# Optimization experiments

Hardware: AMD Instinct MI355X
Metric: run time of the kernel (lower is better)

The kernel has to match this reference:

```python
import jax, jax.numpy as jnp
import numpy as np

B, S, E, D, H, L = 128, 50, 512, 1024, 16, 4
V, NU, NF, NR = 100000, 50000, 10000, 5
DK = D // H
FF = 4 * D


def _pe(S, D):
    # FranchisePositionalEncoding: two interleaved sin/cos halves (chrono + release*1.5)
    half = D // 2
    pos = jnp.arange(S, dtype=jnp.float32)[:, None]
    div = jnp.exp(jnp.arange(0, half, 2, dtype=jnp.float32) * (-np.log(10000.0) / half))
    def il(a):
        return jnp.stack([jnp.sin(a), jnp.cos(a)], axis=-1).reshape(S, half)
    return jnp.concatenate([il(pos * div), il(pos * div * 1.5)], axis=-1)  # [S, D]


def _ln(x, g, b):
    m = x.mean(-1, keepdims=True)
    v = ((x - m) ** 2).mean(-1, keepdims=True)
    return (x - m) * jax.lax.rsqrt(v + 1e-5) * g + b


def _gelu(x):
    return jax.nn.gelu(x, approximate=False)


def setup_inputs() -> dict:
    key = jax.random.key(0)
    ks = iter(jax.random.split(key, 64))
    def p(shape, s=0.02):
        return jax.random.normal(next(ks), shape, jnp.float32) * s
    inp = {
        'movie_table': p((V, E)), 'fran_table': p((NF, E)), 'entry_table': p((NR, E)),
        'proj_w': p((3 * E, D)), 'proj_b': jnp.zeros((D,), jnp.float32),
        'wq': p((L, D, D)), 'bq': jnp.zeros((L, D), jnp.float32),
        'wk': p((L, D, D)), 'bk': jnp.zeros((L, D), jnp.float32),
        'wv': p((L, D, D)), 'bv': jnp.zeros((L, D), jnp.float32),
        'wo': p((L, D, D)), 'bo': jnp.zeros((L, D), jnp.float32),
        'rel_table': p((L, NR, DK)),
        'aln_g': jnp.ones((L, D), jnp.float32), 'aln_b': jnp.zeros((L, D), jnp.float32),
        'f_w1': p((L, D, FF)), 'f_b1': jnp.zeros((L, FF), jnp.float32),
        'f_w2': p((L, FF, D)), 'f_b2': jnp.zeros((L, D), jnp.float32),
        'ln_g': jnp.ones((L, D), jnp.float32), 'ln_b': jnp.zeros((L, D), jnp.float32),
        'user_table': p((NU, D)),
        'mq_w': p((D, D)), 'mq_b': jnp.zeros((D,), jnp.float32),
        'mk_w': p((D, D)), 'mk_b': jnp.zeros((D,), jnp.float32),
        'mv_w': p((D, D)), 'mv_b': jnp.zeros((D,), jnp.float32),
        'mo_w': p((D, D)), 'mo_b': jnp.zeros((D,), jnp.float32),
        'c_w1': p((2 * D, D)), 'c_b1': jnp.zeros((D,), jnp.float32),
        'c_w2': p((D, 1)), 'c_b2': jnp.zeros((1,), jnp.float32),
        'n_w1': p((2 * D, D)), 'n_b1': jnp.zeros((D,), jnp.float32),
        'n_w2': p((D, V)), 'n_b2': jnp.zeros((V,), jnp.float32),
        'r_w1': p((3 * D, D)), 'r_b1': jnp.zeros((D,), jnp.float32),
        'r_w2': p((D, 1)), 'r_b2': jnp.zeros((1,), jnp.float32),
        'o_w1': p((D, D // 2)), 'o_b1': jnp.zeros((D // 2,), jnp.float32),
        'o_w2': p((D // 2, 2)), 'o_b2': jnp.zeros((2,), jnp.float32),
        'user_ids': jax.random.randint(next(ks), (B,), 0, NU),
        'movie_ids': jax.random.randint(next(ks), (B, S), 0, V),
        'franchise_ids': jax.random.randint(next(ks), (B, S), 0, NF),
        'entry_types': jax.random.randint(next(ks), (B, S), 0, NR),
        'relation_matrix': jax.random.randint(next(ks), (S, S), 0, NR),
    }
    return inp


def reference(movie_table, fran_table, entry_table, proj_w, proj_b,
              wq, bq, wk, bk, wv, bv, wo, bo, rel_table, aln_g, aln_b,
              f_w1, f_b1, f_w2, f_b2, ln_g, ln_b, user_table,
              mq_w, mq_b, mk_w, mk_b, mv_w, mv_b, mo_w, mo_b,
              c_w1, c_b1, c_w2, c_b2, n_w1, n_b1, n_w2, n_b2,
              r_w1, r_b1, r_w2, r_b2, o_w1, o_b1, o_w2, o_b2,
              user_ids, movie_ids, franchise_ids, entry_types, relation_matrix):
    b, s = movie_ids.shape
    d = proj_w.shape[1]
    nl, _, dk = rel_table.shape
    h = d // dk
    scale = 1.0 / np.sqrt(dk).astype(np.float32)

    # encoder input: concat(movie, franchise, entry) embeddings -> proj -> +PE
    x = jnp.concatenate([movie_table[movie_ids], fran_table[franchise_ids],
                         entry_table[entry_types]], axis=-1) @ proj_w + proj_b
    x = x + _pe(s, d)

    for l in range(nl):
        res = x
        q = (x @ wq[l] + bq[l]).reshape(b, s, h, dk).transpose(0, 2, 1, 3)  # [b,h,s,dk]
        k = (x @ wk[l] + bk[l]).reshape(b, s, h, dk).transpose(0, 2, 1, 3)
        v = (x @ wv[l] + bv[l]).reshape(b, s, h, dk).transpose(0, 2, 1, 3)
        scores = jnp.einsum('bhid,bhjd->bhij', q, k) * scale
        rel = rel_table[l][relation_matrix]  # [s,s,dk]
        scores = scores + 0.5 * jnp.einsum('bhid,ijd->bhij', q, rel)
        attn = jax.nn.softmax(scores, axis=-1)
        ctx = jnp.einsum('bhij,bhjd->bhid', attn, v).transpose(0, 2, 1, 3).reshape(b, s, d)
        x = _ln(ctx @ wo[l] + bo[l] + res, aln_g[l], aln_b[l])
        ff = _gelu(x @ f_w1[l] + f_b1[l]) @ f_w2[l] + f_b2[l]
        x = _ln(x + ff, ln_g[l], ln_b[l])

    # user preference cross-attention (nn.MultiheadAttention, q_len=1)
    user_emb = user_table[user_ids]  # [b,d]
    qh = (user_emb @ mq_w + mq_b).reshape(b, h, dk)
    kh = (x @ mk_w + mk_b).reshape(b, s, h, dk)
    vh = (x @ mv_w + mv_b).reshape(b, s, h, dk)
    a = jax.nn.softmax(jnp.einsum('bhd,bshd->bhs', qh, kh) * scale, axis=-1)
    user_pref = jnp.einsum('bhs,bshd->bhd', a, vh).reshape(b, d) @ mo_w + mo_b

    seq_repr = x.mean(axis=1)  # mask is None path
    ci = jnp.concatenate([user_pref, seq_repr], axis=-1)
    completion = jax.nn.sigmoid(_gelu(ci @ c_w1 + c_b1) @ c_w2 + c_b2)
    next_logits = _gelu(ci @ n_w1 + n_b1) @ n_w2 + n_b2
    ri = jnp.concatenate([user_emb, user_pref, seq_repr], axis=-1)
    rating = _gelu(ri @ r_w1 + r_b1) @ r_w2 + r_b2
    order = jax.nn.softmax(_gelu(user_pref @ o_w1 + o_b1) @ o_w2 + o_b2, axis=-1)
    return (x, completion, next_logits, rating, order, user_pref)
```

## Files before the change

kernel.cpp:

```cpp
#include <hip/hip_runtime.h>
#include <hip/hip_bf16.h>
#include <math.h>

#define B_   128
#define S_   50
#define BS_  (B_*S_)
#define E_   512
#define D_   1024
#define H_   16
#define DK_  64
#define L_   4
#define FF_  4096
#define V_   100000

typedef short bf8_t __attribute__((ext_vector_type(8)));
typedef float f32x4 __attribute__((ext_vector_type(4)));
typedef unsigned short u16;

__device__ __forceinline__ float gelu_exact(float x) {
    return 0.5f * x * (1.0f + erff(x * 0.70710678118654752440f));
}
__device__ __forceinline__ u16 f2bf(float f) {
    unsigned int u = __float_as_uint(f);
    return (u16)((u + 0x7FFFu + ((u >> 16) & 1u)) >> 16);
}
__device__ __forceinline__ float bf2f(u16 u) {
    return __uint_as_float(((unsigned int)u) << 16);
}

__device__ __forceinline__ void gload16(const u16* g, u16* l) {
    auto* g1 = reinterpret_cast<const __attribute__((address_space(1))) unsigned int*>(
                   reinterpret_cast<uintptr_t>(g));
    auto* l3 = reinterpret_cast<__attribute__((address_space(3))) unsigned int*>(
                   reinterpret_cast<uintptr_t>(l));
    __builtin_amdgcn_global_load_lds(g1, l3, 16, 0, 0);
}

__device__ __forceinline__ void wtrans_body(
    const float* __restrict__ W, u16* __restrict__ Wt,
    int K, int N, int nb, int kb, int dstRowOff)
{
    __shared__ float t[32][33];
    int c = threadIdx.x & 31, r0 = threadIdx.x >> 5;
    #pragma unroll
    for (int rr = 0; rr < 32; rr += 8)
        t[rr + r0][c] = W[(size_t)(kb + rr + r0) * N + nb + c];
    __syncthreads();
    #pragma unroll
    for (int rr = 0; rr < 32; rr += 8)
        Wt[(size_t)(dstRowOff + nb + rr + r0) * K + kb + c] = f2bf(t[c][rr + r0]);
}

__global__ __launch_bounds__(256) void wtrans(
    const float* __restrict__ W, u16* __restrict__ Wt,
    int K, int N, long srcLS, long dstLS, int dstRowOff)
{
    int l = blockIdx.z;
    wtrans_body(W + (size_t)l * srcLS, Wt + (size_t)l * dstLS,
                K, N, blockIdx.x * 32, blockIdx.y * 32, dstRowOff);
}

__global__ __launch_bounds__(256) void wtrans_qkv(
    const float* __restrict__ wq, const float* __restrict__ wk, const float* __restrict__ wv,
    u16* __restrict__ dst)
{
    int z = blockIdx.z;
    int l = z & 3, which = z >> 2;
    const float* W = (which == 0 ? wq : which == 1 ? wk : wv) + (size_t)l * (D_ * D_);
    u16* Wt = dst + (size_t)l * (3 * D_ * D_) + (size_t)which * (D_ * D_);
    wtrans_body(W, Wt, D_, D_, blockIdx.x * 32, blockIdx.y * 32, 0);
}

struct WT8 { const float* s[8]; u16* d[8]; };
__global__ __launch_bounds__(256) void wtrans8(WT8 p)
{
    int z = blockIdx.z;
    wtrans_body(p.s[z], p.d[z], D_, D_, blockIdx.x * 32, blockIdx.y * 32, 0);
}

__global__ __launch_bounds__(256) void wtrans_ff(
    const float* __restrict__ w1, const float* __restrict__ w2,
    u16* __restrict__ d1, u16* __restrict__ d2)
{
    if (blockIdx.z == 0)
        wtrans_body(w1, d1, D_, FF_, blockIdx.x * 32, blockIdx.y * 32, 0);
    else
        wtrans_body(w2, d2, FF_, D_, blockIdx.y * 32, blockIdx.x * 32, 0);
}

__global__ __launch_bounds__(256) void embed_concat(
    const float* __restrict__ mt, const float* __restrict__ ft, const float* __restrict__ et,
    const int* __restrict__ mids, const int* __restrict__ fids, const int* __restrict__ eids,
    u16* __restrict__ xinb)
{
    int bs = blockIdx.x;
    int mid = mids[bs], fid = fids[bs], eid = eids[bs];
    const float* srcs[3] = { mt + (size_t)mid * E_, ft + (size_t)fid * E_, et + (size_t)eid * E_ };
    u16* dst = xinb + (size_t)bs * (3 * E_);
    for (int i = threadIdx.x; i < 384; i += 256) {
        int seg = i >> 7, off = i & 127;
        float4 v = reinterpret_cast<const float4*>(srcs[seg])[off];
        ushort4 b;
        b.x = f2bf(v.x); b.y = f2bf(v.y); b.z = f2bf(v.z); b.w = f2bf(v.w);
        reinterpret_cast<ushort4*>(dst + seg * E_)[off] = b;
    }
}

__global__ __launch_bounds__(256) void setup_misc(
    const float* __restrict__ bq, const float* __restrict__ bk, const float* __restrict__ bv,
    const float* __restrict__ cb1, const float* __restrict__ nb1,
    const float* __restrict__ mkb, const float* __restrict__ mvb,
    float* __restrict__ bqkv, float* __restrict__ bcn, float* __restrict__ bkv,
    float* __restrict__ pet)
{
    int bi = blockIdx.x, tid = threadIdx.x;
    if (bi < 4) {
        for (int c = tid; c < 3072; c += 256) {
            float v = (c < 1024) ? bq[bi * 1024 + c]
                    : (c < 2048) ? bk[bi * 1024 + c - 1024]
                                 : bv[bi * 1024 + c - 2048];
            bqkv[bi * 3072 + c] = v;
        }
    } else if (bi == 4) {
        for (int c = tid; c < 2048; c += 256)
            bcn[c] = (c < 1024) ? cb1[c] : nb1[c - 1024];
    } else if (bi == 5) {
        for (int c = tid; c < 2048; c += 256)
            bkv[c] = (c < 1024) ? mkb[c] : mvb[c - 1024];
    } else {
        int s = bi - 6;
        const float cc = -logf(10000.0f) / 512.0f;
        for (int d = tid; d < D_; d += 256) {
            int second = d >= 512;
            int c2 = second ? d - 512 : d;
            int i = c2 >> 1;
            float div = expf(cc * (float)(2 * i));
            float aa = (float)s * div * (second ? 1.5f : 1.0f);
            pet[s * D_ + d] = (c2 & 1) ? cosf(aa) : sinf(aa);
        }
    }
}

template<int BM>
__global__ __launch_bounds__(256) void gemm_bf16_t(
    const u16* __restrict__ A, int lda, const u16* __restrict__ Wt,
    const float* __restrict__ bias, float* __restrict__ Cf,
    u16* __restrict__ Cb, int ldcb, u16* __restrict__ Cb2, int ldcb2,
    int N, int K, int act, const float* __restrict__ pe)
{
    constexpr int MR   = BM / 32;
    constexpr int AL   = BM / 64;
    constexpr int ABUF = BM * 32;
    __shared__ u16 As[2 * ABUF];
    __shared__ u16 Bs[2 * 4096];
    const int tid  = threadIdx.x;
    const int lane = tid & 63;
    const int wid  = tid >> 6;
    const int wr   = wid >> 1, wc = wid & 1;

    const int gx  = gridDim.x;
    const int nwg = gx * gridDim.y;
    int orig = blockIdx.y * gx + blockIdx.x;
    int qq = nwg >> 3, rr2 = nwg & 7, xcd = orig & 7, idx = orig >> 3;
    int wgid = (xcd < rr2) ? (xcd * (qq + 1) + idx)
                           : (rr2 * (qq + 1) + (xcd - rr2) * qq + idx);
    const int rowBase = (wgid / gx) * BM;
    const int colBase = (wgid % gx) * 128;

    const int fr = lane & 15;
    const int hi = lane >> 4;

    const int sRowL  = lane >> 2;
    const int sChunk = lane & 3;
    const int aRow0 = wid * (BM / 4) + sRowL;
    const int aKey  = (aRow0 >> 1) & 3;
    const u16* aS0 = A + (size_t)(rowBase + aRow0) * lda + ((sChunk ^ aKey) << 3);
    const u16* aS1 = aS0 + (size_t)16 * lda;
    const int ldsA0 = (wid * (BM / 4)) * 32;
    const int ldsA1 = ldsA0 + 512;
    const int bRow0 = wid * 32 + sRowL;
    const int bKey  = (bRow0 >> 1) & 3;
    const u16* bS0 = Wt + (size_t)(colBase + bRow0) * K + ((sChunk ^ bKey) << 3);
    const u16* bS1 = bS0 + (size_t)16 * K;
    const int ldsB0 = (wid * 32) * 32;
    const int ldsB1 = ldsB0 + 512;

    const int swz = ((hi ^ ((fr >> 1) & 3)) << 3);
    const int aRd = (wr * (BM / 2) + fr) * 32 + swz;
    const int bRd = (wc * 64 + fr) * 32 + swz;

    f32x4 acc[MR][4] = {};
    const int nk = K >> 5;

    auto STAGE = [&](int kb, int buf) {
        u16* dA = As + buf * ABUF;
        u16* dB = Bs + buf * 4096;
        gload16(aS0 + kb, dA + ldsA0);
        if constexpr (AL == 2) gload16(aS1 + kb, dA + ldsA1);
        gload16(bS0 + kb, dB + ldsB0);
        gload16(bS1 + kb, dB + ldsB1);
    };

    STAGE(0, 0);
    __builtin_amdgcn_sched_barrier(0);
    STAGE(32, 1);
    __builtin_amdgcn_sched_barrier(0);
    if constexpr (BM == 128) asm volatile("s_waitcnt vmcnt(4)\n\ts_barrier" ::: "memory");
    else                     asm volatile("s_waitcnt vmcnt(3)\n\ts_barrier" ::: "memory");
    __builtin_amdgcn_sched_barrier(0);

    for (int t = 0; t < nk; ++t) {
        const int cur = t & 1;
        const u16* bA = As + cur * ABUF;
        const u16* bB = Bs + cur * 4096;
        bf8_t af[MR], bf[4];
        #pragma unroll
        for (int m = 0; m < MR; ++m)
            af[m] = *reinterpret_cast<const bf8_t*>(&bA[aRd + m * 512]);
        #pragma unroll
        for (int n = 0; n < 4; ++n)
            bf[n] = *reinterpret_cast<const bf8_t*>(&bB[bRd + n * 512]);
        #pragma unroll
        for (int m = 0; m < MR; ++m)
            #pragma unroll
            for (int n = 0; n < 4; ++n)
                acc[m][n] = __builtin_amdgcn_mfma_f32_16x16x32_bf16(af[m], bf[n], acc[m][n], 0, 0, 0);
        if (t == nk - 1) break;
        __builtin_amdgcn_sched_barrier(0);
        asm volatile("s_waitcnt lgkmcnt(0)\n\ts_barrier" ::: "memory");
        __builtin_amdgcn_sched_barrier(0);
        if (t + 2 < nk) {
            STAGE((t + 2) << 5, cur);
            __builtin_amdgcn_sched_barrier(0);
            if constexpr (BM == 128) asm volatile("s_waitcnt vmcnt(4)\n\ts_barrier" ::: "memory");
            else                     asm volatile("s_waitcnt vmcnt(3)\n\ts_barrier" ::: "memory");
        } else {
            asm volatile("s_waitcnt vmcnt(0)\n\ts_barrier" ::: "memory");
        }
        __builtin_amdgcn_sched_barrier(0);
    }

    const int orow = hi << 2;
    #pragma unroll
    for (int m = 0; m < MR; ++m) {
        int r0 = rowBase + wr * (BM / 2) + m * 16 + orow;
        #pragma unroll
        for (int n = 0; n < 4; ++n) {
            int c = colBase + wc * 64 + n * 16 + fr;
            float bv = bias ? bias[c] : 0.0f;
            #pragma unroll
            for (int r = 0; r < 4; ++r) {
                float v = acc[m][n][r] + bv;
                if (act == 1) v = gelu_exact(v);
                if (pe) v += pe[(size_t)((r0 + r) % S_) * N + c];
                if (Cf)  Cf [(size_t)(r0 + r) * N + c] = v;
                if (Cb)  Cb [(size_t)(r0 + r) * ldcb  + c] = f2bf(v);
                if (Cb2) Cb2[(size_t)(r0 + r) * ldcb2 + c] = f2bf(v);
            }
        }
    }
}

__global__ __launch_bounds__(256) void gemm_sk(
    const u16* __restrict__ A, int lda, const u16* __restrict__ Wt, int ldb,
    float* __restrict__ P0, float* __restrict__ P1,
    int N, int Kh)
{
    __shared__ u16 As[2 * 4096];
    __shared__ u16 Bs[2 * 4096];
    const int tid  = threadIdx.x;
    const int lane = tid & 63;
    const int wid  = tid >> 6;
    const int wr   = wid >> 1, wc = wid & 1;

    const int gx  = gridDim.x;
    const int nwg = gx * gridDim.y;
    int orig = blockIdx.y * gx + blockIdx.x;
    int qq = nwg >> 3, rr2 = nwg & 7, xcd = orig & 7, idx = orig >> 3;
    int wgid = (xcd < rr2) ? (xcd * (qq + 1) + idx)
                           : (rr2 * (qq + 1) + (xcd - rr2) * qq + idx);
    const int rowBase = (wgid / gx) * 128;
    const int colBase = (wgid % gx) * 128;
    const int k0 = blockIdx.z * Kh;
    float* P = blockIdx.z ? P1 : P0;

    const int fr = lane & 15;
    const int hi = lane >> 4;

    const int sRowL  = lane >> 2;
    const int sChunk = lane & 3;
    const int gRow0  = (wid << 5) + sRowL;
    const int skey   = (gRow0 >> 1) & 3;
    const int gC     = (sChunk ^ skey) << 3;
    const u16* aS0 = A  + (size_t)(rowBase + gRow0) * lda + k0 + gC;
    const u16* aS1 = aS0 + (size_t)16 * lda;
    const u16* bS0 = Wt + (size_t)(colBase + gRow0) * ldb + k0 + gC;
    const u16* bS1 = bS0 + (size_t)16 * ldb;
    const int ldsW0 = (wid << 5) << 5;
    const int ldsW1 = ldsW0 + (16 << 5);

    const int swz = ((hi ^ ((fr >> 1) & 3)) << 3);
    const int aRd = (wr * 64 + fr) * 32 + swz;
    const int bRd = (wc * 64 + fr) * 32 + swz;

    f32x4 acc[4][4] = {};
    const int nk = Kh >> 5;

    auto STAGE = [&](int kb, int buf) {
        u16* dA = As + buf * 4096;
        u16* dB = Bs + buf * 4096;
        gload16(aS0 + kb, dA + ldsW0);
        gload16(aS1 + kb, dA + ldsW1);
        gload16(bS0 + kb, dB + ldsW0);
        gload16(bS1 + kb, dB + ldsW1);
    };

    STAGE(0, 0);
    __builtin_amdgcn_sched_barrier(0);
    STAGE(32, 1);
    __builtin_amdgcn_sched_barrier(0);
    asm volatile("s_waitcnt vmcnt(4)\n\ts_barrier" ::: "memory");
    __builtin_amdgcn_sched_barrier(0);

    for (int t = 0; t < nk; ++t) {
        const int cur = t & 1;
        const u16* bA = As + cur * 4096;
        const u16* bB = Bs + cur * 4096;
        bf8_t af[4], bf[4];
        #pragma unroll
        for (int m = 0; m < 4; ++m)
            af[m] = *reinterpret_cast<const bf8_t*>(&bA[aRd + m * 512]);
        #pragma unroll
        for (int n = 0; n < 4; ++n)
            bf[n] = *reinterpret_cast<const bf8_t*>(&bB[bRd + n * 512]);
        #pragma unroll
        for (int m = 0; m < 4; ++m)
            #pragma unroll
            for (int n = 0; n < 4; ++n)
                acc[m][n] = __builtin_amdgcn_mfma_f32_16x16x32_bf16(af[m], bf[n], acc[m][n], 0, 0, 0);
        if (t == nk - 1) break;
        __builtin_amdgcn_sched_barrier(0);
        asm volatile("s_waitcnt lgkmcnt(0)\n\ts_barrier" ::: "memory");
        __builtin_amdgcn_sched_barrier(0);
        if (t + 2 < nk) {
            STAGE((t + 2) << 5, cur);
            __builtin_amdgcn_sched_barrier(0);
            asm volatile("s_waitcnt vmcnt(4)\n\ts_barrier" ::: "memory");
        } else {
            asm volatile("s_waitcnt vmcnt(0)\n\ts_barrier" ::: "memory");
        }
        __builtin_amdgcn_sched_barrier(0);
    }

    const int orow = hi << 2;
    #pragma unroll
    for (int m = 0; m < 4; ++m) {
        int r0 = rowBase + wr * 64 + m * 16 + orow;
        #pragma unroll
        for (int n = 0; n < 4; ++n) {
            int c = colBase + wc * 64 + n * 16 + fr;
            #pragma unroll
            for (int r = 0; r < 4; ++r)
                P[(size_t)(r0 + r) * N + c] = acc[m][n][r];
        }
    }
}

__global__ __launch_bounds__(256) void combine_bias_pe(
    const float* __restrict__ p1, const float* __restrict__ p2,
    const float* __restrict__ bias, const float* __restrict__ pe,
    u16* __restrict__ outb)
{
    int row = blockIdx.x, tid = threadIdx.x;
    int c0 = tid << 2;
    size_t base = (size_t)row * D_ + c0;
    float4 v1 = *reinterpret_cast<const float4*>(p1 + base);
    float4 v2 = *reinterpret_cast<const float4*>(p2 + base);
    float4 bv = *reinterpret_cast<const float4*>(bias + c0);
    float4 pv = *reinterpret_cast<const float4*>(pe + (size_t)(row % S_) * D_ + c0);
    ushort4 ob;
    ob.x = f2bf(v1.x + v2.x + bv.x + pv.x);
    ob.y = f2bf(v1.y + v2.y + bv.y + pv.y);
    ob.z = f2bf(v1.z + v2.z + bv.z + pv.z);
    ob.w = f2bf(v1.w + v2.w + bv.w + pv.w);
    *reinterpret_cast<ushort4*>(outb + base) = ob;
}

__global__ __launch_bounds__(256) void add_ln2(
    const float* __restrict__ p1, const float* __restrict__ p2,
    const float* __restrict__ bias, const u16* __restrict__ res,
    const float* __restrict__ g, const float* __restrict__ be,
    u16* __restrict__ outb, float* __restrict__ outf)
{
    int row = blockIdx.x, tid = threadIdx.x;
    int c0 = tid << 2;
    size_t base = (size_t)row * D_ + c0;
    float4 v1 = *reinterpret_cast<const float4*>(p1 + base);
    float4 v2 = *reinterpret_cast<const float4*>(p2 + base);
    float4 bv = *reinterpret_cast<const float4*>(bias + c0);
    ushort4 vr = *reinterpret_cast<const ushort4*>(res + base);
    float vals[4] = { v1.x + v2.x + bv.x + bf2f(vr.x),
                      v1.y + v2.y + bv.y + bf2f(vr.y),
                      v1.z + v2.z + bv.z + bf2f(vr.z),
                      v1.w + v2.w + bv.w + bf2f(vr.w) };
    float s = vals[0] + vals[1] + vals[2] + vals[3];
    __shared__ float red[8];
    #pragma unroll
    for (int off = 32; off; off >>= 1) s += __shfl_xor(s, off);
    int wave = tid >> 6, lane = tid & 63;
    if (lane == 0) red[wave] = s;
    __syncthreads();
    float mean = (red[0] + red[1] + red[2] + red[3]) * (1.0f / D_);
    float vv = 0.0f;
    #pragma unroll
    for (int t = 0; t < 4; ++t) {
        float d = vals[t] - mean;
        vv += d * d;
    }
    #pragma unroll
    for (int off = 32; off; off >>= 1) vv += __shfl_xor(vv, off);
    if (lane == 0) red[4 + wave] = vv;
    __syncthreads();
    float var = (red[4] + red[5] + red[6] + red[7]) * (1.0f / D_);
    float rstd = rsqrtf(var + 1e-5f);
    float4 gv  = *reinterpret_cast<const float4*>(g  + c0);
    float4 bev = *reinterpret_cast<const float4*>(be + c0);
    float o0 = (vals[0] - mean) * rstd * gv.x + bev.x;
    float o1 = (vals[1] - mean) * rstd * gv.y + bev.y;
    float o2 = (vals[2] - mean) * rstd * gv.z + bev.z;
    float o3 = (vals[3] - mean) * rstd * gv.w + bev.w;
    ushort4 ob;
    ob.x = f2bf(o0); ob.y = f2bf(o1); ob.z = f2bf(o2); ob.w = f2bf(o3);
    *reinterpret_cast<ushort4*>(outb + base) = ob;
    if (outf) {
        float4 of = { o0, o1, o2, o3 };
        *reinterpret_cast<float4*>(outf + base) = of;
    }
}

__global__ __launch_bounds__(256) void gemm_logits(
    const float* __restrict__ A, int lda, const float* __restrict__ W,
    const float* __restrict__ bias, float* __restrict__ C, int N, int K)
{
    __shared__ u16 As[2][128][40];
    __shared__ u16 Bs[2][128][40];
    const int tid  = threadIdx.x;
    const int lane = tid & 63;
    const int wid  = tid >> 6;
    const int wr   = wid >> 1, wc = wid & 1;
    const int colBase = blockIdx.x * 128;

    const int a_r = tid >> 1;
    const int a_h = (tid & 1) << 4;
    const int b_c = tid & 127;
    const int b_h = (tid >> 7) << 4;

    const int fr = lane & 15;
    const int fk = (lane >> 4) << 3;

    f32x4 acc[4][4] = {};
    const int nvalid = N - colBase;
    const bool valid = b_c < nvalid;
    const int nk = K >> 5;

    float4 aR[4];
    float  bR[16];

    auto LD = [&](int kb) {
        const float* Ap = A + (size_t)a_r * lda + kb + a_h;
        #pragma unroll
        for (int q = 0; q < 4; ++q)
            aR[q] = *reinterpret_cast<const float4*>(Ap + q * 4);
        const float* Wp = W + (size_t)(kb + b_h) * N + colBase + b_c;
        #pragma unroll
        for (int kk = 0; kk < 16; ++kk)
            bR[kk] = valid ? Wp[(size_t)kk * N] : 0.0f;
    };
    auto ST = [&](int buf) {
        #pragma unroll
        for (int q = 0; q < 4; ++q) {
            ushort4 bb;
            bb.x = f2bf(aR[q].x); bb.y = f2bf(aR[q].y);
            bb.z = f2bf(aR[q].z); bb.w = f2bf(aR[q].w);
            *reinterpret_cast<ushort4*>(&As[buf][a_r][a_h + q * 4]) = bb;
        }
        u16 tmp[16];
        #pragma unroll
        for (int kk = 0; kk < 16; ++kk) tmp[kk] = f2bf(bR[kk]);
        *reinterpret_cast<bf8_t*>(&Bs[buf][b_c][b_h])     = *reinterpret_cast<const bf8_t*>(tmp);
        *reinterpret_cast<bf8_t*>(&Bs[buf][b_c][b_h + 8]) = *reinterpret_cast<const bf8_t*>(tmp + 8);
    };

    LD(0); ST(0);
    __syncthreads();

    for (int t = 0; t < nk; ++t) {
        if (t + 1 < nk) LD((t + 1) << 5);
        const int cur = t & 1;
        bf8_t af[4], bfv[4];
        #pragma unroll
        for (int m = 0; m < 4; ++m)
            af[m] = *reinterpret_cast<const bf8_t*>(&As[cur][wr * 64 + m * 16 + fr][fk]);
        #pragma unroll
        for (int n = 0; n < 4; ++n)
            bfv[n] = *reinterpret_cast<const bf8_t*>(&Bs[cur][wc * 64 + n * 16 + fr][fk]);
        #pragma unroll
        for (int m = 0; m < 4; ++m)
            #pragma unroll
            for (int n = 0; n < 4; ++n)
                acc[m][n] = __builtin_amdgcn_mfma_f32_16x16x32_bf16(af[m], bfv[n], acc[m][n], 0, 0, 0);
        if (t + 1 < nk) ST(cur ^ 1);
        __syncthreads();
    }

    const int orow = (lane >> 4) << 2;
    #pragma unroll
    for (int m = 0; m < 4; ++m) {
        int r0 = wr * 64 + m * 16 + orow;
        #pragma unroll
// ... 179 lines not shown
    const float* proj_w      = (const float*)d_in[3];
    const float* proj_b      = (const float*)d_in[4];
    const float* wq          = (const float*)d_in[5];
    const float* bq          = (const float*)d_in[6];
    const float* wk          = (const float*)d_in[7];
    const float* bk          = (const float*)d_in[8];
    const float* wv          = (const float*)d_in[9];
    const float* bv          = (const float*)d_in[10];
    const float* wo          = (const float*)d_in[11];
    const float* bo          = (const float*)d_in[12];
    const float* rel_table   = (const float*)d_in[13];
    const float* aln_g       = (const float*)d_in[14];
    const float* aln_b       = (const float*)d_in[15];
    const float* f_w1        = (const float*)d_in[16];
    const float* f_b1        = (const float*)d_in[17];
    const float* f_w2        = (const float*)d_in[18];
    const float* f_b2        = (const float*)d_in[19];
    const float* ln_g        = (const float*)d_in[20];
    const float* ln_b        = (const float*)d_in[21];
    const float* user_table  = (const float*)d_in[22];
    const float* mq_w        = (const float*)d_in[23];
    const float* mq_b        = (const float*)d_in[24];
    const float* mk_w        = (const float*)d_in[25];
    const float* mk_b        = (const float*)d_in[26];
    const float* mv_w        = (const float*)d_in[27];
    const float* mv_b        = (const float*)d_in[28];
    const float* mo_w        = (const float*)d_in[29];
    const float* mo_b        = (const float*)d_in[30];
    const float* c_w1        = (const float*)d_in[31];
    const float* c_b1        = (const float*)d_in[32];
    const float* c_w2        = (const float*)d_in[33];
    const float* c_b2        = (const float*)d_in[34];
    const float* n_w1        = (const float*)d_in[35];
    const float* n_b1        = (const float*)d_in[36];
    const float* n_w2        = (const float*)d_in[37];
    const float* n_b2        = (const float*)d_in[38];
    const float* r_w1        = (const float*)d_in[39];
    const float* r_b1        = (const float*)d_in[40];
    const float* r_w2        = (const float*)d_in[41];
    const float* r_b2        = (const float*)d_in[42];
    const float* o_w1        = (const float*)d_in[43];
    const float* o_b1        = (const float*)d_in[44];
    const float* o_w2        = (const float*)d_in[45];
    const float* o_b2        = (const float*)d_in[46];
    const int* user_ids      = (const int*)d_in[47];
    const int* movie_ids     = (const int*)d_in[48];
    const int* franchise_ids = (const int*)d_in[49];
    const int* entry_types   = (const int*)d_in[50];
    const int* relation_mat  = (const int*)d_in[51];

    u16* up16 = (u16*)d_ws;
    u16* proj_wt = up16;
    u16* wqkv_t  = proj_wt + (size_t)1024 * 1536;
    u16* wo_t    = wqkv_t  + (size_t)4 * 3072 * 1024;
    u16* fw1_buf = wo_t    + (size_t)4 * 1024 * 1024;
    u16* fw2_buf = fw1_buf + (size_t)4096 * 1024;
    u16* mq_t    = fw2_buf + (size_t)1024 * 4096;
    u16* mk_t    = mq_t    + (size_t)1024 * 1024;
    u16* mv_t    = mk_t    + (size_t)1024 * 1024;
    u16* mo_t    = mv_t    + (size_t)1024 * 1024;
    u16* cn_w1t  = mo_t    + (size_t)1024 * 1024;
    u16* r_w1t   = cn_w1t  + (size_t)2048 * 2048;
    u16* o_w1t   = r_w1t   + (size_t)1024 * 3072;
    u16* ffb     = o_w1t   + (size_t)512 * 1024;
    u16* xinb    = ffb;
    u16* xb      = ffb     + (size_t)BS_ * FF_;
    u16* xb2     = xb      + (size_t)BS_ * D_;
    u16* qkvb    = xb2     + (size_t)BS_ * D_;
    u16* kvb     = qkvb    + (size_t)BS_ * 3 * D_;
    u16* ctxb    = kvb;
    u16* ueb     = kvb     + (size_t)BS_ * 2 * D_;
    u16* upb_pre = ueb     + (size_t)B_ * D_;
    u16* cib     = upb_pre + (size_t)B_ * D_;
    u16* rib     = cib     + (size_t)B_ * 2 * D_;
    float* fp    = (float*)(rib + (size_t)B_ * 3 * D_);
    float* bqkv  = fp;
    float* bcn   = bqkv + 4 * 3072;
    float* bkv   = bcn  + 2048;
    float* pet   = bkv  + 2048;
    float* h1cn  = pet  + 50 * 1024;
    float* h1r   = h1cn + (size_t)B_ * 2048;
    float* ho    = h1r  + (size_t)B_ * D_;

    float* pQK = (float*)qkvb;
    float* pKV = (float*)kvb;
    float* pFF = (float*)ffb;

    float* xout    = (float*)d_out;
    float* comp    = xout + (size_t)BS_ * D_;
    float* logits  = comp + B_;
    float* rating  = logits + (size_t)B_ * V_;
    float* order   = rating + B_;
    float* upref   = order + 2 * B_;

    dim3 blk(256);

    wtrans<<<dim3(32, 48, 1), blk, 0, stream>>>(proj_w, proj_wt, 1536, 1024, 0, 0, 0);
    wtrans_qkv<<<dim3(32, 32, 12), blk, 0, stream>>>(wq, wk, wv, wqkv_t);
    WT8 w8;
    w8.s[0] = wo;                 w8.d[0] = wo_t;
    w8.s[1] = wo + 1048576;       w8.d[1] = wo_t + 1048576;
    w8.s[2] = wo + 2097152;       w8.d[2] = wo_t + 2097152;
    w8.s[3] = wo + 3145728;       w8.d[3] = wo_t + 3145728;
    w8.s[4] = mq_w;               w8.d[4] = mq_t;
    w8.s[5] = mk_w;               w8.d[5] = mk_t;
    w8.s[6] = mv_w;               w8.d[6] = mv_t;
    w8.s[7] = mo_w;               w8.d[7] = mo_t;
    wtrans8<<<dim3(32, 32, 8), blk, 0, stream>>>(w8);
    wtrans<<<dim3(32, 64, 1), blk, 0, stream>>>(c_w1, cn_w1t, 2048, 1024, 0, 0, 0);
    wtrans<<<dim3(32, 64, 1), blk, 0, stream>>>(n_w1, cn_w1t, 2048, 1024, 0, 0, 1024);
    wtrans<<<dim3(32, 96, 1), blk, 0, stream>>>(r_w1, r_w1t, 3072, 1024, 0, 0, 0);
    wtrans<<<dim3(16, 32, 1), blk, 0, stream>>>(o_w1, o_w1t, 1024, 512, 0, 0, 0);
    setup_misc<<<dim3(56), blk, 0, stream>>>(bq, bk, bv, c_b1, n_b1, mk_b, mv_b,
                                             bqkv, bcn, bkv, pet);

    embed_concat<<<BS_, blk, 0, stream>>>(movie_table, fran_table, entry_table,
                                          movie_ids, franchise_ids, entry_types, xinb);
    gemm_sk<<<dim3(8, 50, 2), blk, 0, stream>>>(xinb, 1536, proj_wt, 1536,
                                                pQK, pKV, D_, 768);
    combine_bias_pe<<<BS_, blk, 0, stream>>>(pQK, pKV, proj_b, pet, xb);

    for (int l = 0; l < L_; ++l) {
        gemm_bf16_t<128><<<dim3(24, 50), blk, 0, stream>>>(xb, 1024,
                wqkv_t + (size_t)l * 3145728, bqkv + l * 3072,
                nullptr, qkvb, 3072, nullptr, 0, 3 * D_, D_, 0, nullptr);
        attn_kernel<<<B_ * H_, blk, 0, stream>>>(qkvb, rel_table + (size_t)l * 5 * DK_,
                                                 relation_mat, ctxb);
        gemm_sk<<<dim3(8, 50, 2), blk, 0, stream>>>(ctxb, 1024,
                wo_t + (size_t)l * 1048576, 1024, pQK, pFF, D_, 512);
        add_ln2<<<BS_, blk, 0, stream>>>(pQK, pFF, bo + l * D_, xb,
                                         aln_g + l * D_, aln_b + l * D_, xb2, nullptr);
        wtrans_ff<<<dim3(128, 32, 2), blk, 0, stream>>>(f_w1 + (size_t)l * D_ * FF_,
                                                        f_w2 + (size_t)l * FF_ * D_,
                                                        fw1_buf, fw2_buf);
        gemm_bf16_t<128><<<dim3(32, 50), blk, 0, stream>>>(xb2, 1024, fw1_buf, f_b1 + l * FF_,
                nullptr, ffb, 4096, nullptr, 0, FF_, D_, 1, nullptr);
        gemm_sk<<<dim3(8, 50, 2), blk, 0, stream>>>(ffb, 4096, fw2_buf, 4096,
                                                    pQK, pKV, D_, 2048);
        add_ln2<<<BS_, blk, 0, stream>>>(pQK, pKV, f_b2 + l * D_, xb2,
                                         ln_g + l * D_, ln_b + l * D_, xb,
                                         (l == L_ - 1) ? xout : nullptr);
    }

    gather_user<<<B_, blk, 0, stream>>>(user_table, user_ids, ueb, 1024, rib, 3072);
    gemm_bf16_t<64><<<dim3(8, 2), blk, 0, stream>>>(ueb, 1024, mq_t, mq_b,
            nullptr, qkvb, 1024, nullptr, 0, D_, D_, 0, nullptr);
    gemm_bf16_t<128><<<dim3(16, 50), blk, 0, stream>>>(xb, 1024, mk_t, bkv,
            nullptr, kvb, 2048, nullptr, 0, 2 * D_, D_, 0, nullptr);
    cross_attn<<<B_ * H_, dim3(64), 0, stream>>>(qkvb, kvb, upb_pre);
    gemm_bf16_t<64><<<dim3(8, 2), blk, 0, stream>>>(upb_pre, 1024, mo_t, mo_b,
            upref, cib, 2048, rib + 1024, 3072, D_, D_, 0, nullptr);

    seq_mean<<<B_, blk, 0, stream>>>(xout, cib + 1024, 2048, rib + 2048, 3072);

    gemm_bf16_t<64><<<dim3(16, 2), blk, 0, stream>>>(cib, 2048, cn_w1t, bcn,
            h1cn, nullptr, 0, nullptr, 0, 2048, 2048, 1, nullptr);
    gemm_bf16_t<64><<<dim3(8, 2), blk, 0, stream>>>(rib, 3072, r_w1t, r_b1,
            h1r, nullptr, 0, nullptr, 0, D_, 3072, 1, nullptr);
    gemm_bf16_t<64><<<dim3(4, 2), blk, 0, stream>>>(cib, 2048, o_w1t, o_b1,
            ho, nullptr, 0, nullptr, 0, 512, D_, 1, nullptr);
    gemm_logits<<<dim3(782, 1), blk, 0, stream>>>(h1cn + 1024, 2048, n_w2, n_b2,
                                                  logits, V_, D_);
    heads_final<<<B_, blk, 0, stream>>>(h1cn, h1r, ho, c_w2, c_b2, r_w2, r_b2,
                                        o_w2, o_b2, comp, rating, order);
}
```

Baseline: 2.192 ms.

## Switch large GEMMs to 32x32x16 MFMA and store split-K partials as bf16

The large 128x128 GEMMs (QKV, FFN1, cross-attention K/V) and the split-K GEMMs now use the 32x32x16 bf16 MFMA with 2x2 f32x16 accumulators and a matching LDS read swizzle, in place of 4x4 tiles of 16x16x32. The 32x32 instruction covers the same work with fewer MFMA issues and fewer LDS fragment reads per K-step. The split-K partial sums are now written as bf16 instead of f32, halving the partial-sum traffic in gemm_sk32, combine_bias_pe and add_ln2, at the cost of extra rounding error before the bias, residual and layernorm. The small-M gemm_bf16_t path drops the XCD remapping and the unused pe argument.

```diff
diff --git a/kernel.cpp b/kernel.cpp
--- a/kernel.cpp
+++ b/kernel.cpp
@@ -15,6 +15,7 @@
 
 typedef short bf8_t __attribute__((ext_vector_type(8)));
 typedef float f32x4 __attribute__((ext_vector_type(4)));
+typedef float f32x16 __attribute__((ext_vector_type(16)));
 typedef unsigned short u16;
 
 __device__ __forceinline__ float gelu_exact(float x) {
@@ -141,17 +142,13 @@
     }
 }
 
-template<int BM>
-__global__ __launch_bounds__(256) void gemm_bf16_t(
+__global__ __launch_bounds__(256) void gemm128_w32(
     const u16* __restrict__ A, int lda, const u16* __restrict__ Wt,
-    const float* __restrict__ bias, float* __restrict__ Cf,
-    u16* __restrict__ Cb, int ldcb, u16* __restrict__ Cb2, int ldcb2,
-    int N, int K, int act, const float* __restrict__ pe)
-{
-    constexpr int MR   = BM / 32;
-    constexpr int AL   = BM / 64;
-    constexpr int ABUF = BM * 32;
-    __shared__ u16 As[2 * ABUF];
+    const float* __restrict__ bias,
+    u16* __restrict__ Cb, int ldcb,
+    int N, int K, int act)
+{
+    __shared__ u16 As[2 * 4096];
     __shared__ u16 Bs[2 * 4096];
     const int tid  = threadIdx.x;
     const int lane = tid & 63;
@@ -164,67 +161,70 @@
     int qq = nwg >> 3, rr2 = nwg & 7, xcd = orig & 7, idx = orig >> 3;
     int wgid = (xcd < rr2) ? (xcd * (qq + 1) + idx)
                            : (rr2 * (qq + 1) + (xcd - rr2) * qq + idx);
-    const int rowBase = (wgid / gx) * BM;
+    const int rowBase = (wgid / gx) * 128;
     const int colBase = (wgid % gx) * 128;
-
-    const int fr = lane & 15;
-    const int hi = lane >> 4;
 
     const int sRowL  = lane >> 2;
     const int sChunk = lane & 3;
-    const int aRow0 = wid * (BM / 4) + sRowL;
-    const int aKey  = (aRow0 >> 1) & 3;
-    const u16* aS0 = A + (size_t)(rowBase + aRow0) * lda + ((sChunk ^ aKey) << 3);
+    const int gRow0  = (wid << 5) + sRowL;
+    const int skey   = (gRow0 >> 1) & 3;
+    const int gC     = (sChunk ^ skey) << 3;
+    const u16* aS0 = A  + (size_t)(rowBase + gRow0) * lda + gC;
     const u16* aS1 = aS0 + (size_t)16 * lda;
-    const int ldsA0 = (wid * (BM / 4)) * 32;
-    const int ldsA1 = ldsA0 + 512;
-    const int bRow0 = wid * 32 + sRowL;
-    const int bKey  = (bRow0 >> 1) & 3;
-    const u16* bS0 = Wt + (size_t)(colBase + bRow0) * K + ((sChunk ^ bKey) << 3);
+    const u16* bS0 = Wt + (size_t)(colBase + gRow0) * K + gC;
     const u16* bS1 = bS0 + (size_t)16 * K;
-    const int ldsB0 = (wid * 32) * 32;
-    const int ldsB1 = ldsB0 + 512;
-
-    const int swz = ((hi ^ ((fr >> 1) & 3)) << 3);
-    const int aRd = (wr * (BM / 2) + fr) * 32 + swz;
-    const int bRd = (wc * 64 + fr) * 32 + swz;
-
-    f32x4 acc[MR][4] = {};
+    const int ldsW0 = (wid << 5) << 5;
+    const int ldsW1 = ldsW0 + (16 << 5);
+
+    const int l31 = lane & 31;
+    const int hi5 = lane >> 5;
+    const int key32 = (l31 >> 1) & 3;
+    const int c0 = (0 | hi5) ^ key32;
+    const int c1 = (2 | hi5) ^ key32;
+    const int aB0 = (wr * 64 + l31) * 32;
+    const int bB0 = (wc * 64 + l31) * 32;
+
+    f32x16 acc[2][2] = {};
     const int nk = K >> 5;
 
     auto STAGE = [&](int kb, int buf) {
-        u16* dA = As + buf * ABUF;
+        u16* dA = As + buf * 4096;
         u16* dB = Bs + buf * 4096;
-        gload16(aS0 + kb, dA + ldsA0);
-        if constexpr (AL == 2) gload16(aS1 + kb, dA + ldsA1);
-        gload16(bS0 + kb, dB + ldsB0);
-        gload16(bS1 + kb, dB + ldsB1);
+        gload16(aS0 + kb, dA + ldsW0);
+        gload16(aS1 + kb, dA + ldsW1);
+        gload16(bS0 + kb, dB + ldsW0);
+        gload16(bS1 + kb, dB + ldsW1);
     };
 
     STAGE(0, 0);
     __builtin_amdgcn_sched_barrier(0);
     STAGE(32, 1);
     __builtin_amdgcn_sched_barrier(0);
-    if constexpr (BM == 128) asm volatile("s_waitcnt vmcnt(4)\n\ts_barrier" ::: "memory");
-    else                     asm volatile("s_waitcnt vmcnt(3)\n\ts_barrier" ::: "memory");
+    asm volatile("s_waitcnt vmcnt(4)\n\ts_barrier" ::: "memory");
     __builtin_amdgcn_sched_barrier(0);
 
     for (int t = 0; t < nk; ++t) {
         const int cur = t & 1;
-        const u16* bA = As + cur * ABUF;
+        const u16* bA = As + cur * 4096;
         const u16* bB = Bs + cur * 4096;
-        bf8_t af[MR], bf[4];
-        #pragma unroll
-        for (int m = 0; m < MR; ++m)
-            af[m] = *reinterpret_cast<const bf8_t*>(&bA[aRd + m * 512]);
-        #pragma unroll
-        for (int n = 0; n < 4; ++n)
-            bf[n] = *reinterpret_cast<const bf8_t*>(&bB[bRd + n * 512]);
-        #pragma unroll
-        for (int m = 0; m < MR; ++m)
+        bf8_t aF[2][2], bF[2][2];
+        #pragma unroll
+        for (int mi = 0; mi < 2; ++mi) {
+            aF[mi][0] = *reinterpret_cast<const bf8_t*>(&bA[aB0 + mi * 1024 + c0 * 8]);
+            aF[mi][1] = *reinterpret_cast<const bf8_t*>(&bA[aB0 + mi * 1024 + c1 * 8]);
+        }
+        #pragma unroll
+        for (int ni = 0; ni < 2; ++ni) {
+            bF[ni][0] = *reinterpret_cast<const bf8_t*>(&bB[bB0 + ni * 1024 + c0 * 8]);
+            bF[ni][1] = *reinterpret_cast<const bf8_t*>(&bB[bB0 + ni * 1024 + c1 * 8]);
+        }
+        #pragma unroll
+        for (int mi = 0; mi < 2; ++mi)
             #pragma unroll
-            for (int n = 0; n < 4; ++n)
-                acc[m][n] = __builtin_amdgcn_mfma_f32_16x16x32_bf16(af[m], bf[n], acc[m][n], 0, 0, 0);
+            for (int ni = 0; ni < 2; ++ni) {
+                acc[mi][ni] = __builtin_amdgcn_mfma_f32_32x32x16_bf16(aF[mi][0], bF[ni][0], acc[mi][ni], 0, 0, 0);
+                acc[mi][ni] = __builtin_amdgcn_mfma_f32_32x32x16_bf16(aF[mi][1], bF[ni][1], acc[mi][ni], 0, 0, 0);
+            }
         if (t == nk - 1) break;
         __builtin_amdgcn_sched_barrier(0);
         asm volatile("s_waitcnt lgkmcnt(0)\n\ts_barrier" ::: "memory");
@@ -232,38 +232,34 @@
         if (t + 2 < nk) {
             STAGE((t + 2) << 5, cur);
             __builtin_amdgcn_sched_barrier(0);
-            if constexpr (BM == 128) asm volatile("s_waitcnt vmcnt(4)\n\ts_barrier" ::: "memory");
-            else                     asm volatile("s_waitcnt vmcnt(3)\n\ts_barrier" ::: "memory");
+            asm volatile("s_waitcnt vmcnt(4)\n\ts_barrier" ::: "memory");
         } else {
             asm volatile("s_waitcnt vmcnt(0)\n\ts_barrier" ::: "memory");
         }
         __builtin_amdgcn_sched_barrier(0);
     }
 
-    const int orow = hi << 2;
-    #pragma unroll
-    for (int m = 0; m < MR; ++m) {
-        int r0 = rowBase + wr * (BM / 2) + m * 16 + orow;
-        #pragma unroll
-        for (int n = 0; n < 4; ++n) {
-            int c = colBase + wc * 64 + n * 16 + fr;
-            float bv = bias ? bias[c] : 0.0f;
+    #pragma unroll
+    for (int mi = 0; mi < 2; ++mi) {
+        int rt = rowBase + wr * 64 + mi * 32 + 4 * hi5;
+        #pragma unroll
+        for (int ni = 0; ni < 2; ++ni) {
+            int ct = colBase + wc * 64 + ni * 32 + l31;
+            float bv = bias ? bias[ct] : 0.0f;
             #pragma unroll
-            for (int r = 0; r < 4; ++r) {
-                float v = acc[m][n][r] + bv;
+            for (int r = 0; r < 16; ++r) {
+                int rr = rt + (r & 3) + 8 * (r >> 2);
+                float v = acc[mi][ni][r] + bv;
                 if (act == 1) v = gelu_exact(v);
-                if (pe) v += pe[(size_t)((r0 + r) % S_) * N + c];
-                if (Cf)  Cf [(size_t)(r0 + r) * N + c] = v;
-                if (Cb)  Cb [(size_t)(r0 + r) * ldcb  + c] = f2bf(v);
-                if (Cb2) Cb2[(size_t)(r0 + r) * ldcb2 + c] = f2bf(v);
+                Cb[(size_t)rr * ldcb + ct] = f2bf(v);
             }
         }
     }
 }
 
-__global__ __launch_bounds__(256) void gemm_sk(
+__global__ __launch_bounds__(256) void gemm_sk32(
     const u16* __restrict__ A, int lda, const u16* __restrict__ Wt, int ldb,
-    float* __restrict__ P0, float* __restrict__ P1,
+    u16* __restrict__ P0, u16* __restrict__ P1,
     int N, int Kh)
 {
     __shared__ u16 As[2 * 4096];
@@ -282,10 +278,7 @@
     const int rowBase = (wgid / gx) * 128;
     const int colBase = (wgid % gx) * 128;
     const int k0 = blockIdx.z * Kh;
-    float* P = blockIdx.z ? P1 : P0;
-
-    const int fr = lane & 15;
-    const int hi = lane >> 4;
+    u16* P = blockIdx.z ? P1 : P0;
 
     const int sRowL  = lane >> 2;
     const int sChunk = lane & 3;
@@ -299,11 +292,15 @@
     const int ldsW0 = (wid << 5) << 5;
     const int ldsW1 = ldsW0 + (16 << 5);
 
-    const int swz = ((hi ^ ((fr >> 1) & 3)) << 3);
-    const int aRd = (wr * 64 + fr) * 32 + swz;
-    const int bRd = (wc * 64 + fr) * 32 + swz;
-
-    f32x4 acc[4][4] = {};
+    const int l31 = lane & 31;
+    const int hi5 = lane >> 5;
+    const int key32 = (l31 >> 1) & 3;
+    const int c0 = (0 | hi5) ^ key32;
+    const int c1 = (2 | hi5) ^ key32;
+    const int aB0 = (wr * 64 + l31) * 32;
+    const int bB0 = (wc * 64 + l31) * 32;
+
+    f32x16 acc[2][2] = {};
     const int nk = Kh >> 5;
 
     auto STAGE = [&](int kb, int buf) {
@@ -326,18 +323,24 @@
         const int cur = t & 1;
         const u16* bA = As + cur * 4096;
         const u16* bB = Bs + cur * 4096;
-        bf8_t af[4], bf[4];
-        #pragma unroll
-        for (int m = 0; m < 4; ++m)
-            af[m] = *reinterpret_cast<const bf8_t*>(&bA[aRd + m * 512]);
-        #pragma unroll
-        for (int n = 0; n < 4; ++n)
-            bf[n] = *reinterpret_cast<const bf8_t*>(&bB[bRd + n * 512]);
-        #pragma unroll
-        for (int m = 0; m < 4; ++m)
+        bf8_t aF[2][2], bF[2][2];
+        #pragma unroll
+        for (int mi = 0; mi < 2; ++mi) {
+            aF[mi][0] = *reinterpret_cast<const bf8_t*>(&bA[aB0 + mi * 1024 + c0 * 8]);
+            aF[mi][1] = *reinterpret_cast<const bf8_t*>(&bA[aB0 + mi * 1024 + c1 * 8]);
+        }
+        #pragma unroll
+        for (int ni = 0; ni < 2; ++ni) {
+            bF[ni][0] = *reinterpret_cast<const bf8_t*>(&bB[bB0 + ni * 1024 + c0 * 8]);
+            bF[ni][1] = *reinterpret_cast<const bf8_t*>(&bB[bB0 + ni * 1024 + c1 * 8]);
+        }
+        #pragma unroll
+        for (int mi = 0; mi < 2; ++mi)
             #pragma unroll
-            for (int n = 0; n < 4; ++n)
-                acc[m][n] = __builtin_amdgcn_mfma_f32_16x16x32_bf16(af[m], bf[n], acc[m][n], 0, 0, 0);
+            for (int ni = 0; ni < 2; ++ni) {
+                acc[mi][ni] = __builtin_amdgcn_mfma_f32_32x32x16_bf16(aF[mi][0], bF[ni][0], acc[mi][ni], 0, 0, 0);
+                acc[mi][ni] = __builtin_amdgcn_mfma_f32_32x32x16_bf16(aF[mi][1], bF[ni][1], acc[mi][ni], 0, 0, 0);
+            }
         if (t == nk - 1) break;
         __builtin_amdgcn_sched_barrier(0);
         asm volatile("s_waitcnt lgkmcnt(0)\n\ts_barrier" ::: "memory");
@@ -352,42 +355,43 @@
         __builtin_amdgcn_sched_barrier(0);
     }
 
-    const int orow = hi << 2;
-    #pragma unroll
-    for (int m = 0; m < 4; ++m) {
-        int r0 = rowBase + wr * 64 + m * 16 + orow;
-        #pragma unroll
-        for (int n = 0; n < 4; ++n) {
-            int c = colBase + wc * 64 + n * 16 + fr;
+    #pragma unroll
+    for (int mi = 0; mi < 2; ++mi) {
+        int rt = rowBase + wr * 64 + mi * 32 + 4 * hi5;
+        #pragma unroll
+        for (int ni = 0; ni < 2; ++ni) {
+            int ct = colBase + wc * 64 + ni * 32 + l31;
             #pragma unroll
-            for (int r = 0; r < 4; ++r)
-                P[(size_t)(r0 + r) * N + c] = acc[m][n][r];
+            for (int r = 0; r < 16; ++r) {
+                int rr = rt + (r & 3) + 8 * (r >> 2);
+                P[(size_t)rr * N + ct] = f2bf(acc[mi][ni][r]);
+            }
         }
     }
 }
 
 __global__ __launch_bounds__(256) void combine_bias_pe(
-    const float* __restrict__ p1, const float* __restrict__ p2,
+    const u16* __restrict__ p1, const u16* __restrict__ p2,
     const float* __restrict__ bias, const float* __restrict__ pe,
     u16* __restrict__ outb)
 {
     int row = blockIdx.x, tid = threadIdx.x;
     int c0 = tid << 2;
     size_t base = (size_t)row * D_ + c0;
-    float4 v1 = *reinterpret_cast<const float4*>(p1 + base);
-    float4 v2 = *reinterpret_cast<const float4*>(p2 + base);
+    ushort4 v1 = *reinterpret_cast<const ushort4*>(p1 + base);
+    ushort4 v2 = *reinterpret_cast<const ushort4*>(p2 + base);
     float4 bv = *reinterpret_cast<const float4*>(bias + c0);
     float4 pv = *reinterpret_cast<const float4*>(pe + (size_t)(row % S_) * D_ + c0);
     ushort4 ob;
-    ob.x = f2bf(v1.x + v2.x + bv.x + pv.x);
-    ob.y = f2bf(v1.y + v2.y + bv.y + pv.y);
-    ob.z = f2bf(v1.z + v2.z + bv.z + pv.z);
-    ob.w = f2bf(v1.w + v2.w + bv.w + pv.w);
+    ob.x = f2bf(bf2f(v1.x) + bf2f(v2.x) + bv.x + pv.x);
+    ob.y = f2bf(bf2f(v1.y) + bf2f(v2.y) + bv.y + pv.y);
+    ob.z = f2bf(bf2f(v1.z) + bf2f(v2.z) + bv.z + pv.z);
+    ob.w = f2bf(bf2f(v1.w) + bf2f(v2.w) + bv.w + pv.w);
     *reinterpret_cast<ushort4*>(outb + base) = ob;
 }
 
 __global__ __launch_bounds__(256) void add_ln2(
-    const float* __restrict__ p1, const float* __restrict__ p2,
+    const u16* __restrict__ p1, const u16* __restrict__ p2,
     const float* __restrict__ bias, const u16* __restrict__ res,
     const float* __restrict__ g, const float* __restrict__ be,
     u16* __restrict__ outb, float* __restrict__ outf)
@@ -395,14 +399,14 @@
     int row = blockIdx.x, tid = threadIdx.x;
     int c0 = tid << 2;
     size_t base = (size_t)row * D_ + c0;
-    float4 v1 = *reinterpret_cast<const float4*>(p1 + base);
-    float4 v2 = *reinterpret_cast<const float4*>(p2 + base);
+    ushort4 v1 = *reinterpret_cast<const ushort4*>(p1 + base);
+    ushort4 v2 = *reinterpret_cast<const ushort4*>(p2 + base);
     float4 bv = *reinterpret_cast<const float4*>(bias + c0);
     ushort4 vr = *reinterpret_cast<const ushort4*>(res + base);
-    float vals[4] = { v1.x + v2.x + bv.x + bf2f(vr.x),
-                      v1.y + v2.y + bv.y + bf2f(vr.y),
-                      v1.z + v2.z + bv.z + bf2f(vr.z),
-                      v1.w + v2.w + bv.w + bf2f(vr.w) };
+    float vals[4] = { bf2f(v1.x) + bf2f(v2.x) + bv.x + bf2f(vr.x),
+                      bf2f(v1.y) + bf2f(v2.y) + bv.y + bf2f(vr.y),
+                      bf2f(v1.z) + bf2f(v2.z) + bv.z + bf2f(vr.z),
+                      bf2f(v1.w) + bf2f(v2.w) + bv.w + bf2f(vr.w) };
     float s = vals[0] + vals[1] + vals[2] + vals[3];
     __shared__ float red[8];
     #pragma unroll
@@ -435,6 +439,119 @@
     if (outf) {
         float4 of = { o0, o1, o2, o3 };
         *reinterpret_cast<float4*>(outf + base) = of;
+    }
+}
+
+template<int BM>
+__global__ __launch_bounds__(256) void gemm_bf16_t(
+    const u16* __restrict__ A, int lda, const u16* __restrict__ Wt,
+    const float* __restrict__ bias, float* __restrict__ Cf,
+    u16* __restrict__ Cb, int ldcb, u16* __restrict__ Cb2, int ldcb2,
+    int N, int K, int act)
+{
+    constexpr int MR   = BM / 32;
+    constexpr int AL   = BM / 64;
+    constexpr int ABUF = BM * 32;
+    __shared__ u16 As[2 * ABUF];
+    __shared__ u16 Bs[2 * 4096];
+    const int tid  = threadIdx.x;
+    const int lane = tid & 63;
+    const int wid  = tid >> 6;
+    const int wr   = wid >> 1, wc = wid & 1;
+
+    const int rowBase = blockIdx.y * BM;
+    const int colBase = blockIdx.x * 128;
+
+    const int fr = lane & 15;
+    const int hi = lane >> 4;
+
+    const int sRowL  = lane >> 2;
+    const int sChunk = lane & 3;
+    const int aRow0 = wid * (BM / 4) + sRowL;
+    const int aKey  = (aRow0 >> 1) & 3;
+    const u16* aS0 = A + (size_t)(rowBase + aRow0) * lda + ((sChunk ^ aKey) << 3);
+    const u16* aS1 = aS0 + (size_t)16 * lda;
+    const int ldsA0 = (wid * (BM / 4)) * 32;
+    const int ldsA1 = ldsA0 + 512;
+    const int bRow0 = wid * 32 + sRowL;
+    const int bKey  = (bRow0 >> 1) & 3;
+    const u16* bS0 = Wt + (size_t)(colBase + bRow0) * K + ((sChunk ^ bKey) << 3);
+    const u16* bS1 = bS0 + (size_t)16 * K;
+    const int ldsB0 = (wid * 32) * 32;
+    const int ldsB1 = ldsB0 + 512;
+
+    const int swz = ((hi ^ ((fr >> 1) & 3)) << 3);
+    const int aRd = (wr * (BM / 2) + fr) * 32 + swz;
+    const int bRd = (wc * 64 + fr) * 32 + swz;
+
+    f32x4 acc[MR][4] = {};
+    const int nk = K >> 5;
+
+    auto STAGE = [&](int kb, int buf) {
+        u16* dA = As + buf * ABUF;
+        u16* dB = Bs + buf * 4096;
+        gload16(aS0 + kb, dA + ldsA0);
+        if constexpr (AL == 2) gload16(aS1 + kb, dA + ldsA1);
+        gload16(bS0 + kb, dB + ldsB0);
+        gload16(bS1 + kb, dB + ldsB1);
+    };
+
+    STAGE(0, 0);
+    __builtin_amdgcn_sched_barrier(0);
+    STAGE(32, 1);
+    __builtin_amdgcn_sched_barrier(0);
+    if constexpr (BM == 128) asm volatile("s_waitcnt vmcnt(4)\n\ts_barrier" ::: "memory");
+    else                     asm volatile("s_waitcnt vmcnt(3)\n\ts_barrier" ::: "memory");
+    __builtin_amdgcn_sched_barrier(0);
+
+    for (int t = 0; t < nk; ++t) {
+        const int cur = t & 1;
+        const u16* bA = As + cur * ABUF;
+        const u16* bB = Bs + cur * 4096;
+        bf8_t af[MR], bf[4];
+        #pragma unroll
+        for (int m = 0; m < MR; ++m)
+            af[m] = *reinterpret_cast<const bf8_t*>(&bA[aRd + m * 512]);
+        #pragma unroll
+        for (int n = 0; n < 4; ++n)
+            bf[n] = *reinterpret_cast<const bf8_t*>(&bB[bRd + n * 512]);
+        #pragma unroll
+        for (int m = 0; m < MR; ++m)
+            #pragma unroll
+            for (int n = 0; n < 4; ++n)
+                acc[m][n] = __builtin_amdgcn_mfma_f32_16x16x32_bf16(af[m], bf[n], acc[m][n], 0, 0, 0);
+        if (t == nk - 1) break;
+        __builtin_amdgcn_sched_barrier(0);
+        asm volatile("s_waitcnt lgkmcnt(0)\n\ts_barrier" ::: "memory");
+        __builtin_amdgcn_sched_barrier(0);
+        if (t + 2 < nk) {
+            STAGE((t + 2) << 5, cur);
+            __builtin_amdgcn_sched_barrier(0);
+            if constexpr (BM == 128) asm volatile("s_waitcnt vmcnt(4)\n\ts_barrier" ::: "memory");
+            else                     asm volatile("s_waitcnt vmcnt(3)\n\ts_barrier" ::: "memory");
+        } else {
+            asm volatile("s_waitcnt vmcnt(0)\n\ts_barrier" ::: "memory");
+        }
+        __builtin_amdgcn_sched_barrier(0);
+    }
+
+    const int orow = hi << 2;
+    #pragma unroll
+    for (int m = 0; m < MR; ++m) {
+        int r0 = rowBase + wr * (BM / 2) + m * 16 + orow;
+        #pragma unroll
+        for (int n = 0; n < 4; ++n) {
+            int c = colBase + wc * 64 + n * 16 + fr;
+            float bv = bias ? bias[c] : 0.0f;
+            #pragma unroll
+            for (int r = 0; r < 4; ++r) {
+                float v = acc[m][n][r] + bv;
+                if (act == 1) v = gelu_exact(v);
+                if (Cf)  Cf [(size_t)(r0 + r) * N + c] = v;
+                if (Cb)  Cb [(size_t)(r0 + r) * ldcb  + c] = f2bf(v);
+                if (Cb2) Cb2[(size_t)(r0 + r) * ldcb2 + c] = f2bf(v);
+            }
+        }
     }
 }
 
@@ -780,9 +897,9 @@
     float* h1r   = h1cn + (size_t)B_ * 2048;
     float* ho    = h1r  + (size_t)B_ * D_;
 
-    float* pQK = (float*)qkvb;
-    float* pKV = (float*)kvb;
-    float* pFF = (float*)ffb;
+    u16* pQK = qkvb;
+    u16* pKV = kvb;
+    u16* pFF = ffb;
 
     float* xout    = (float*)d_out;
     float* comp    = xout + (size_t)BS_ * D_;
@@ -814,27 +931,27 @@
 
     embed_concat<<<BS_, blk, 0, stream>>>(movie_table, fran_table, entry_table,
                                           movie_ids, franchise_ids, entry_types, xinb);
-    gemm_sk<<<dim3(8, 50, 2), blk, 0, stream>>>(xinb, 1536, proj_wt, 1536,
-                                                pQK, pKV, D_, 768);
+    gemm_sk32<<<dim3(8, 50, 2), blk, 0, stream>>>(xinb, 1536, proj_wt, 1536,
+                                                  pQK, pKV, D_, 768);
     combine_bias_pe<<<BS_, blk, 0, stream>>>(pQK, pKV, proj_b, pet, xb);
 
     for (int l = 0; l < L_; ++l) {
-        gemm_bf16_t<128><<<dim3(24, 50), blk, 0, stream>>>(xb, 1024,
+        gemm128_w32<<<dim3(24, 50), blk, 0, stream>>>(xb, 1024,
                 wqkv_t + (size_t)l * 3145728, bqkv + l * 3072,
-                nullptr, qkvb, 3072, nullptr, 0, 3 * D_, D_, 0, nullptr);
+                qkvb, 3072, 3 * D_, D_, 0);
         attn_kernel<<<B_ * H_, blk, 0, stream>>>(qkvb, rel_table + (size_t)l * 5 * DK_,
                                                  relation_mat, ctxb);
-        gemm_sk<<<dim3(8, 50, 2), blk, 0, stream>>>(ctxb, 1024,
+        gemm_sk32<<<dim3(8, 50, 2), blk, 0, stream>>>(ctxb, 1024,
                 wo_t + (size_t)l * 1048576, 1024, pQK, pFF, D_, 512);
         add_ln2<<<BS_, blk, 0, stream>>>(pQK, pFF, bo + l * D_, xb,
                                          aln_g + l * D_, aln_b + l * D_, xb2, nullptr);
         wtrans_ff<<<dim3(128, 32, 2), blk, 0, stream>>>(f_w1 + (size_t)l * D_ * FF_,
                                                         f_w2 + (size_t)l * FF_ * D_,
                                                         fw1_buf, fw2_buf);
-        gemm_bf16_t<128><<<dim3(32, 50), blk, 0, stream>>>(xb2, 1024, fw1_buf, f_b1 + l * FF_,
-                nullptr, ffb, 4096, nullptr, 0, FF_, D_, 1, nullptr);
-        gemm_sk<<<dim3(8, 50, 2), blk, 0, stream>>>(ffb, 4096, fw2_buf, 4096,
-                                                    pQK, pKV, D_, 2048);
+        gemm128_w32<<<dim3(32, 50), blk, 0, stream>>>(xb2, 1024, fw1_buf, f_b1 + l * FF_,
+                ffb, 4096, FF_, D_, 1);
+        gemm_sk32<<<dim3(8, 50, 2), blk, 0, stream>>>(ffb, 4096, fw2_buf, 4096,
+                                                      pQK, pKV, D_, 2048);
         add_ln2<<<BS_, blk, 0, stream>>>(pQK, pKV, f_b2 + l * D_, xb2,
                                          ln_g + l * D_, ln_b + l * D_, xb,
                                          (l == L_ - 1) ? xout : nullptr);
@@ -842,21 +959,21 @@
 
     gather_user<<<B_, blk, 0, stream>>>(user_table, user_ids, ueb, 1024, rib, 3072);
     gemm_bf16_t<64><<<dim3(8, 2), blk, 0, stream>>>(ueb, 1024, mq_t, mq_b,
-            nullptr, qkvb, 1024, nullptr, 0, D_, D_, 0, nullptr);
-    gemm_bf16_t<128><<<dim3(16, 50), blk, 0, stream>>>(xb, 1024, mk_t, bkv,
-            nullptr, kvb, 2048, nullptr, 0, 2 * D_, D_, 0, nullptr);
+            nullptr, qkvb, 1024, nullptr, 0, D_, D_, 0);
+    gemm128_w32<<<dim3(16, 50), blk, 0, stream>>>(xb, 1024, mk_t, bkv,
+            kvb, 2048, 2 * D_, D_, 0);
     cross_attn<<<B_ * H_, dim3(64), 0, stream>>>(qkvb, kvb, upb_pre);
     gemm_bf16_t<64><<<dim3(8, 2), blk, 0, stream>>>(upb_pre, 1024, mo_t, mo_b,
-            upref, cib, 2048, rib + 1024, 3072, D_, D_, 0, nullptr);
+            upref, cib, 2048, rib + 1024, 3072, D_, D_, 0);
 
     seq_mean<<<B_, blk, 0, stream>>>(xout, cib + 1024, 2048, rib + 2048, 3072);
 
     gemm_bf16_t<64><<<dim3(16, 2), blk, 0, stream>>>(cib, 2048, cn_w1t, bcn,
-            h1cn, nullptr, 0, nullptr, 0, 2048, 2048, 1, nullptr);
+            h1cn, nullptr, 0, nullptr, 0, 2048, 2048, 1);
     gemm_bf16_t<64><<<dim3(8, 2), blk, 0, stream>>>(rib, 3072, r_w1t, r_b1,
-            h1r, nullptr, 0, nullptr, 0, D_, 3072, 1, nullptr);
+            h1r, nullptr, 0, nullptr, 0, D_, 3072, 1);
     gemm_bf16_t<64><<<dim3(4, 2), blk, 0, stream>>>(cib, 2048, o_w1t, o_b1,
-            ho, nullptr, 0, nullptr, 0, 512, D_, 1, nullptr);
+            ho, nullptr, 0, nullptr, 0, 512, D_, 1);
     gemm_logits<<<dim3(782, 1), blk, 0, stream>>>(h1cn + 1024, 2048, n_w2, n_b2,
                                                   logits, V_, D_);
     heads_final<<<B_, blk, 0, stream>>>(h1cn, h1r, ho, c_w2, c_b2, r_w2, r_b2,
```

New measurement: 2.130 ms. -2.8%, faster.
